# Kernel optimization log

Measured on AMD Instinct MI355X. Metric: run time of the kernel, lower is better.

## Reference

```python
import jax, jax.numpy as jnp
import numpy as np
import math

N = 5000
H, W = 512, 512
CHUNK = 100                 # gaussians per scan step; CHUNK*H*W ~ 26M floats
ALPHA_THRESH = 1.0 / 255.0  # same skip threshold as the CUDA rasterizer
TWO_PI = 2.0 * math.pi


def setup_inputs() -> dict:
    key = jax.random.key(0)
    k1, k2, k3, k4 = jax.random.split(key, 4)
    return {
        "_xyz": jax.random.normal(k1, (N, 2), dtype=jnp.float32),
        "_scaling": jax.random.uniform(k2, (N, 2), dtype=jnp.float32),
        "_rotation": jax.random.uniform(k3, (N, 1), dtype=jnp.float32),
        "_features_dc": jax.random.uniform(k4, (N, 3), dtype=jnp.float32),
        "_opacity": jnp.ones((N, 1), dtype=jnp.float32),
    }


def _render(_xyz, _scaling, _rotation, _features_dc, _opacity):
    # --- parameter activations (GaussianImage_RS getters) ---
    means = jnp.tanh(_xyz)                          # [N,2] in (-1,1)
    scale = jnp.abs(_scaling + 0.5)                 # [N,2]  (bound = 0.5)
    theta = jax.nn.sigmoid(_rotation[:, 0]) * TWO_PI

    # --- project_gaussians_2d_scale_rot ---
    # ndc -> pixel centers
    cx = 0.5 * ((means[:, 0] + 1.0) * W - 1.0)      # [N]
    cy = 0.5 * ((means[:, 1] + 1.0) * H - 1.0)
    cth, sth = jnp.cos(theta), jnp.sin(theta)
    sx2 = scale[:, 0] * scale[:, 0]
    sy2 = scale[:, 1] * scale[:, 1]
    # cov2d = R S S^T R^T with R = [[c,-s],[s,c]]
    a = cth * cth * sx2 + sth * sth * sy2
    b = cth * sth * (sx2 - sy2)
    c = sth * sth * sx2 + cth * cth * sy2
    det = a * c - b * b
    valid = det > 0.0
    inv_det = jnp.where(valid, 1.0 / jnp.maximum(det, 1e-12), 0.0)
    A = c * inv_det                                  # conic xx
    B = -b * inv_det                                 # conic xy
    C = a * inv_det                                  # conic yy

    opac = _opacity[:, 0]                            # [N]
    cols = _features_dc                              # [N,3]

    ys, xs = jnp.meshgrid(jnp.arange(H, dtype=jnp.float32),
                          jnp.arange(W, dtype=jnp.float32), indexing="ij")

    # --- rasterize_gaussians_sum: out[p] = sum_i color_i * alpha_i(p) ---
    # scan over gaussian chunks to bound memory (CHUNK x H x W working set)
    def body(acc, g):
        gcx, gcy, gA, gB, gC, gop, gv, gcol = g
        dx = gcx[:, None, None] - xs[None]           # [c,H,W]
        dy = gcy[:, None, None] - ys[None]
        sigma = 0.5 * (gA[:, None, None] * dx * dx
                       + gC[:, None, None] * dy * dy) \
                + gB[:, None, None] * dx * dy
        alpha = gop[:, None, None] * jnp.exp(-sigma)
        alpha = jnp.where((sigma >= 0.0) & (alpha > ALPHA_THRESH)
                          & gv[:, None, None], alpha, 0.0)
        acc = acc + jnp.einsum("chw,ck->hwk", alpha, gcol)
        return acc, None

    def chunked(x):
        return x.reshape(N // CHUNK, CHUNK, *x.shape[1:])

    gauss = tuple(chunked(x) for x in (cx, cy, A, B, C, opac, valid, cols))
    img0 = jnp.zeros((H, W, 3), dtype=jnp.float32)
    img, _ = jax.lax.scan(body, img0, gauss)

    img = jnp.clip(img, 0.0, 1.0)
    # view(-1,H,W,3).permute(0,3,1,2)
    return img.reshape(1, H, W, 3).transpose(0, 3, 1, 2)


def reference(_xyz, _scaling, _rotation, _features_dc, _opacity):
    return _render(_xyz, _scaling, _rotation, _features_dc, _opacity)
```

## Files before the change

### kernel.cpp

```cpp
#include <hip/hip_runtime.h>
#include <math.h>

#define N_G       5000
#define HH        512
#define WW        512
#define TILE      16
#define TDIM      32
#define NTILES    (TDIM * TDIM)
#define GSTRIDE   12
#define PAIR_CAP  (N_G * 8)
#define ALPHA_TH  (1.0f / 255.0f)
#define TWO_PI_F  6.28318530717958647692f

__global__ __launch_bounds__(256) void k_zero(int* counts) {
    int i = blockIdx.x * blockDim.x + threadIdx.x;
    if (i < NTILES) counts[i] = 0;
}

__global__ __launch_bounds__(256) void k_prep(
    const float* __restrict__ xyz, const float* __restrict__ scal,
    const float* __restrict__ rot, const float* __restrict__ fdc,
    const float* __restrict__ opac, float* __restrict__ params,
    int* __restrict__ counts)
{
    int i = blockIdx.x * blockDim.x + threadIdx.x;
    if (i >= N_G) return;

    float mx = tanhf(xyz[2 * i + 0]);
    float my = tanhf(xyz[2 * i + 1]);
    float sx = fabsf(scal[2 * i + 0] + 0.5f);
    float sy = fabsf(scal[2 * i + 1] + 0.5f);
    float th = (1.0f / (1.0f + expf(-rot[i]))) * TWO_PI_F;

    float cx = 0.5f * ((mx + 1.0f) * (float)WW - 1.0f);
    float cy = 0.5f * ((my + 1.0f) * (float)HH - 1.0f);
    float cth = cosf(th), sth = sinf(th);
    float sx2 = sx * sx, sy2 = sy * sy;
    float a = cth * cth * sx2 + sth * sth * sy2;
    float b = cth * sth * (sx2 - sy2);
    float c = sth * sth * sx2 + cth * cth * sy2;
    float det = a * c - b * b;
    bool valid = det > 0.0f;
    float inv_det = valid ? 1.0f / fmaxf(det, 1e-12f) : 0.0f;
    float A = c * inv_det, B = -b * inv_det, C = a * inv_det;
    float op = opac[i];

    float* p = params + (size_t)i * GSTRIDE;
    p[0] = cx; p[1] = cy; p[2] = A; p[3] = B; p[4] = C; p[5] = op;
    p[6] = fdc[3 * i + 0]; p[7] = fdc[3 * i + 1]; p[8] = fdc[3 * i + 2];

    float radius = 0.0f;
    if (valid && op > ALPHA_TH) {
        float tau  = logf(op * 255.0f);
        float mid  = 0.5f * (a + c);
        float rad  = sqrtf(fmaxf(0.0f, 0.25f * (a - c) * (a - c) + b * b));
        float lmax = mid + rad;
        radius = sqrtf(fmaxf(0.0f, 2.0f * tau * lmax)) * 1.0001f + 0.01f;
    }
    p[9] = radius; p[10] = 0.0f; p[11] = 0.0f;

    if (radius > 0.0f) {
        int x0 = max(0,        (int)floorf((cx - radius) * (1.0f / TILE)));
        int x1 = min(TDIM - 1, (int)floorf((cx + radius) * (1.0f / TILE)));
        int y0 = max(0,        (int)floorf((cy - radius) * (1.0f / TILE)));
        int y1 = min(TDIM - 1, (int)floorf((cy + radius) * (1.0f / TILE)));
        for (int ty = y0; ty <= y1; ++ty)
            for (int tx = x0; tx <= x1; ++tx)
                atomicAdd(&counts[ty * TDIM + tx], 1);
    }
}

__global__ __launch_bounds__(1024) void k_scan(
    const int* __restrict__ counts, int* __restrict__ offsets,
    int* __restrict__ cursor)
{
    __shared__ int s[NTILES];
    int tid = threadIdx.x;
    int v0 = counts[tid];
    s[tid] = v0;
    __syncthreads();
    for (int off = 1; off < NTILES; off <<= 1) {
        int v = (tid >= off) ? s[tid - off] : 0;
        __syncthreads();
        s[tid] += v;
        __syncthreads();
    }
    offsets[tid + 1] = s[tid];
    if (tid == 0) offsets[0] = 0;
    cursor[tid] = s[tid] - v0;
}

__global__ __launch_bounds__(256) void k_scatter(
    const float* __restrict__ params, int* __restrict__ cursor,
    int* __restrict__ pairs)
{
    int i = blockIdx.x * blockDim.x + threadIdx.x;
    if (i >= N_G) return;
    const float* p = params + (size_t)i * GSTRIDE;
    float cx = p[0], cy = p[1], radius = p[9];
    if (radius <= 0.0f) return;
    int x0 = max(0,        (int)floorf((cx - radius) * (1.0f / TILE)));
    int x1 = min(TDIM - 1, (int)floorf((cx + radius) * (1.0f / TILE)));
    int y0 = max(0,        (int)floorf((cy - radius) * (1.0f / TILE)));
    int y1 = min(TDIM - 1, (int)floorf((cy + radius) * (1.0f / TILE)));
    for (int ty = y0; ty <= y1; ++ty)
        for (int tx = x0; tx <= x1; ++tx) {
            int pos = atomicAdd(&cursor[ty * TDIM + tx], 1);
            if (pos < PAIR_CAP) pairs[pos] = i;
        }
}

__global__ __launch_bounds__(256) void k_render(
    const float* __restrict__ params, const int* __restrict__ offsets,
    const int* __restrict__ pairs, float* __restrict__ out)
{
    int tx = blockIdx.x, ty = blockIdx.y;
    int t = ty * TDIM + tx;
    int lx = threadIdx.x & (TILE - 1);
    int ly = threadIdx.x >> 4;
    int w = tx * TILE + lx;
    int h = ty * TILE + ly;
    float fx = (float)w, fy = (float)h;

    int s = offsets[t];
    int e = offsets[t + 1];
    if (s > PAIR_CAP) s = PAIR_CAP;
    if (e > PAIR_CAP) e = PAIR_CAP;

    float r0 = 0.0f, r1 = 0.0f, r2 = 0.0f;
    for (int k = s; k < e; ++k) {
        int gi = pairs[k];
        const float* p = params + (size_t)gi * GSTRIDE;
        float dx = p[0] - fx;
        float dy = p[1] - fy;
        float sigma = 0.5f * (p[2] * dx * dx + p[4] * dy * dy) + p[3] * dx * dy;
        float alpha = p[5] * __expf(-sigma);
        bool pass = (sigma >= 0.0f) && (alpha > ALPHA_TH);
        float wgt = pass ? alpha : 0.0f;
        r0 += wgt * p[6];
        r1 += wgt * p[7];
        r2 += wgt * p[8];
    }

    int pix = h * WW + w;
    out[0 * HH * WW + pix] = fminf(fmaxf(r0, 0.0f), 1.0f);
    out[1 * HH * WW + pix] = fminf(fmaxf(r1, 0.0f), 1.0f);
    out[2 * HH * WW + pix] = fminf(fmaxf(r2, 0.0f), 1.0f);
}

extern "C" void kernel_launch(void* const* d_in, const int* in_sizes, int n_in,
                              void* d_out, int out_size, void* d_ws, size_t ws_size,
                              hipStream_t stream) {
    const float* xyz  = (const float*)d_in[0];
    const float* scal = (const float*)d_in[1];
    const float* rot  = (const float*)d_in[2];
    const float* fdc  = (const float*)d_in[3];
    const float* opac = (const float*)d_in[4];
    float* out = (float*)d_out;

    float* params  = (float*)d_ws;
    int*   counts  = (int*)(params + N_G * GSTRIDE);
    int*   offsets = counts + NTILES;
    int*   cursor  = offsets + NTILES + 1;
    int*   pairs   = cursor + NTILES;

    k_zero<<<dim3((NTILES + 255) / 256), dim3(256), 0, stream>>>(counts);
    k_prep<<<dim3((N_G + 255) / 256), dim3(256), 0, stream>>>(
        xyz, scal, rot, fdc, opac, params, counts);
    k_scan<<<dim3(1), dim3(1024), 0, stream>>>(counts, offsets, cursor);
    k_scatter<<<dim3((N_G + 255) / 256), dim3(256), 0, stream>>>(
        params, cursor, pairs);
    k_render<<<dim3(TDIM, TDIM), dim3(256), 0, stream>>>(
        params, offsets, pairs, out);
}
```

Before: 87.19 us.

## Replace global tile binning with per-block shared-memory culling in render kernel

Removes the zero, count, scan and scatter kernels and global pair list. Each render block now tests all 5000 gaussians against its tile bounds and builds a shared-memory list of the ones that overlap, then shades from that list. Gaussian parameters are packed into float4 records for vectorised loads. This cuts three kernel launches and the global atomics, but every block repeats an O(N) cull pass, list order is no longer deterministic, and 20KB of shared memory per block may reduce occupancy.

```diff
diff --git a/kernel.cpp b/kernel.cpp
--- a/kernel.cpp
+++ b/kernel.cpp
@@ -7,21 +7,14 @@
 #define TILE      16
 #define TDIM      32
 #define NTILES    (TDIM * TDIM)
-#define GSTRIDE   12
-#define PAIR_CAP  (N_G * 8)
 #define ALPHA_TH  (1.0f / 255.0f)
 #define TWO_PI_F  6.28318530717958647692f
-
-__global__ __launch_bounds__(256) void k_zero(int* counts) {
-    int i = blockIdx.x * blockDim.x + threadIdx.x;
-    if (i < NTILES) counts[i] = 0;
-}
 
 __global__ __launch_bounds__(256) void k_prep(
     const float* __restrict__ xyz, const float* __restrict__ scal,
     const float* __restrict__ rot, const float* __restrict__ fdc,
-    const float* __restrict__ opac, float* __restrict__ params,
-    int* __restrict__ counts)
+    const float* __restrict__ opac,
+    float4* __restrict__ rec, float4* __restrict__ cull)
 {
     int i = blockIdx.x * blockDim.x + threadIdx.x;
     if (i >= N_G) return;
@@ -45,10 +38,6 @@
     float A = c * inv_det, B = -b * inv_det, C = a * inv_det;
     float op = opac[i];
 
-    float* p = params + (size_t)i * GSTRIDE;
-    p[0] = cx; p[1] = cy; p[2] = A; p[3] = B; p[4] = C; p[5] = op;
-    p[6] = fdc[3 * i + 0]; p[7] = fdc[3 * i + 1]; p[8] = fdc[3 * i + 2];
-
     float radius = 0.0f;
     if (valid && op > ALPHA_TH) {
         float tau  = logf(op * 255.0f);
@@ -57,89 +46,67 @@
         float lmax = mid + rad;
         radius = sqrtf(fmaxf(0.0f, 2.0f * tau * lmax)) * 1.0001f + 0.01f;
     }
-    p[9] = radius; p[10] = 0.0f; p[11] = 0.0f;
 
-    if (radius > 0.0f) {
-        int x0 = max(0,        (int)floorf((cx - radius) * (1.0f / TILE)));
-        int x1 = min(TDIM - 1, (int)floorf((cx + radius) * (1.0f / TILE)));
-        int y0 = max(0,        (int)floorf((cy - radius) * (1.0f / TILE)));
-        int y1 = min(TDIM - 1, (int)floorf((cy + radius) * (1.0f / TILE)));
-        for (int ty = y0; ty <= y1; ++ty)
-            for (int tx = x0; tx <= x1; ++tx)
-                atomicAdd(&counts[ty * TDIM + tx], 1);
-    }
-}
-
-__global__ __launch_bounds__(1024) void k_scan(
-    const int* __restrict__ counts, int* __restrict__ offsets,
-    int* __restrict__ cursor)
-{
-    __shared__ int s[NTILES];
-    int tid = threadIdx.x;
-    int v0 = counts[tid];
-    s[tid] = v0;
-    __syncthreads();
-    for (int off = 1; off < NTILES; off <<= 1) {
-        int v = (tid >= off) ? s[tid - off] : 0;
-        __syncthreads();
-        s[tid] += v;
-        __syncthreads();
-    }
-    offsets[tid + 1] = s[tid];
-    if (tid == 0) offsets[0] = 0;
-    cursor[tid] = s[tid] - v0;
-}
-
-__global__ __launch_bounds__(256) void k_scatter(
-    const float* __restrict__ params, int* __restrict__ cursor,
-    int* __restrict__ pairs)
-{
-    int i = blockIdx.x * blockDim.x + threadIdx.x;
-    if (i >= N_G) return;
-    const float* p = params + (size_t)i * GSTRIDE;
-    float cx = p[0], cy = p[1], radius = p[9];
-    if (radius <= 0.0f) return;
-    int x0 = max(0,        (int)floorf((cx - radius) * (1.0f / TILE)));
-    int x1 = min(TDIM - 1, (int)floorf((cx + radius) * (1.0f / TILE)));
-    int y0 = max(0,        (int)floorf((cy - radius) * (1.0f / TILE)));
-    int y1 = min(TDIM - 1, (int)floorf((cy + radius) * (1.0f / TILE)));
-    for (int ty = y0; ty <= y1; ++ty)
-        for (int tx = x0; tx <= x1; ++tx) {
-            int pos = atomicAdd(&cursor[ty * TDIM + tx], 1);
-            if (pos < PAIR_CAP) pairs[pos] = i;
-        }
+    rec[3 * i + 0] = make_float4(cx, cy, A, B);
+    rec[3 * i + 1] = make_float4(C, op, fdc[3 * i + 0], fdc[3 * i + 1]);
+    rec[3 * i + 2] = make_float4(fdc[3 * i + 2], 0.0f, 0.0f, 0.0f);
+    cull[i]        = make_float4(cx, cy, radius, 0.0f);
 }
 
 __global__ __launch_bounds__(256) void k_render(
-    const float* __restrict__ params, const int* __restrict__ offsets,
-    const int* __restrict__ pairs, float* __restrict__ out)
+    const float4* __restrict__ rec, const float4* __restrict__ cull,
+    float* __restrict__ out)
 {
-    int tx = blockIdx.x, ty = blockIdx.y;
-    int t = ty * TDIM + tx;
+    __shared__ int list[N_G];
+    __shared__ int cnt;
+
+    int t  = blockIdx.x;
+    int tx = t & (TDIM - 1);
+    int ty = t >> 5;
     int lx = threadIdx.x & (TILE - 1);
     int ly = threadIdx.x >> 4;
-    int w = tx * TILE + lx;
-    int h = ty * TILE + ly;
+    int w  = tx * TILE + lx;
+    int h  = ty * TILE + ly;
     float fx = (float)w, fy = (float)h;
 
-    int s = offsets[t];
-    int e = offsets[t + 1];
-    if (s > PAIR_CAP) s = PAIR_CAP;
-    if (e > PAIR_CAP) e = PAIR_CAP;
+    float x0 = (float)(tx * TILE), x1 = (float)(tx * TILE + TILE - 1);
+    float y0 = (float)(ty * TILE), y1 = (float)(ty * TILE + TILE - 1);
+
+    if (threadIdx.x == 0) cnt = 0;
+    __syncthreads();
+
+    for (int base = 0; base < N_G; base += 256) {
+        int i = base + threadIdx.x;
+        if (i < N_G) {
+            float4 q = cull[i];
+            float nx  = fminf(fmaxf(q.x, x0), x1);
+            float ny  = fminf(fmaxf(q.y, y0), y1);
+            float ddx = q.x - nx;
+            float ddy = q.y - ny;
+            if (ddx * ddx + ddy * ddy < q.z * q.z) {
+                int p = atomicAdd(&cnt, 1);
+                list[p] = i;
+            }
+        }
+    }
+    __syncthreads();
+    int e = cnt;
 
     float r0 = 0.0f, r1 = 0.0f, r2 = 0.0f;
-    for (int k = s; k < e; ++k) {
-        int gi = pairs[k];
-        const float* p = params + (size_t)gi * GSTRIDE;
-        float dx = p[0] - fx;
-        float dy = p[1] - fy;
-        float sigma = 0.5f * (p[2] * dx * dx + p[4] * dy * dy) + p[3] * dx * dy;
-        float alpha = p[5] * __expf(-sigma);
+    for (int k = 0; k < e; ++k) {
+        int gi = list[k];
+        float4 pa = rec[3 * gi + 0];
+        float4 pb = rec[3 * gi + 1];
+        float4 pc = rec[3 * gi + 2];
+        float dx = pa.x - fx;
+        float dy = pa.y - fy;
+        float sigma = 0.5f * (pa.z * dx * dx + pb.x * dy * dy) + pa.w * dx * dy;
+        float alpha = pb.y * __expf(-sigma);
         bool pass = (sigma >= 0.0f) && (alpha > ALPHA_TH);
-        float wgt = pass ? alpha : 0.0f;
-        r0 += wgt * p[6];
-        r1 += wgt * p[7];
-        r2 += wgt * p[8];
+        float wg = pass ? alpha : 0.0f;
+        r0 += wg * pb.z;
+        r1 += wg * pb.w;
+        r2 += wg * pc.x;
     }
 
     int pix = h * WW + w;
@@ -158,18 +125,10 @@
     const float* opac = (const float*)d_in[4];
     float* out = (float*)d_out;
 
-    float* params  = (float*)d_ws;
-    int*   counts  = (int*)(params + N_G * GSTRIDE);
-    int*   offsets = counts + NTILES;
-    int*   cursor  = offsets + NTILES + 1;
-    int*   pairs   = cursor + NTILES;
+    float4* rec  = (float4*)d_ws;
+    float4* cull = rec + 3 * N_G;
 
-    k_zero<<<dim3((NTILES + 255) / 256), dim3(256), 0, stream>>>(counts);
     k_prep<<<dim3((N_G + 255) / 256), dim3(256), 0, stream>>>(
-        xyz, scal, rot, fdc, opac, params, counts);
-    k_scan<<<dim3(1), dim3(1024), 0, stream>>>(counts, offsets, cursor);
-    k_scatter<<<dim3((N_G + 255) / 256), dim3(256), 0, stream>>>(
-        params, cursor, pairs);
-    k_render<<<dim3(TDIM, TDIM), dim3(256), 0, stream>>>(
-        params, offsets, pairs, out);
+        xyz, scal, rot, fdc, opac, rec, cull);
+    k_render<<<dim3(NTILES), dim3(256), 0, stream>>>(rec, cull, out);
 }
```

Result: faster. 80.36 us (-7.8%).
